# Performance work log

Measured on AMD Instinct MI355X. Metric: run time of the kernel, lower is better.

The kernel has to match this reference:

```python
import jax, jax.numpy as jnp
import numpy as np

EPS = 1e-5

def conv(x, w, groups=1):
    # x: NCHW, w: OIHW, VALID padding, stride 1 (cross-correlation, same as torch conv2d)
    return jax.lax.conv_general_dilated(x, w, (1, 1), 'VALID',
                                        feature_group_count=groups,
                                        dimension_numbers=('NCHW', 'OIHW', 'NCHW'))

def bn(x, g, b, m, v):
    # eval-mode batchnorm with running stats
    scale = (g / jnp.sqrt(v + EPS))[None, :, None, None]
    return (x - m[None, :, None, None]) * scale + b[None, :, None, None]

def xcorr_depthwise(x, k):
    # x: [B,C,Hs,Ws] search, k: [B,C,Hk,Wk] per-sample kernels
    B, C, H, W = x.shape
    xr = x.reshape(1, B * C, H, W)
    kr = k.reshape(B * C, 1, k.shape[2], k.shape[3])
    out = conv(xr, kr, groups=B * C)  # [1, B*C, Ho, Wo]
    return out.reshape(B, C, out.shape[2], out.shape[3])

def setup_inputs() -> dict:
    key = jax.random.key(0)
    ks = jax.random.split(key, 16)
    Cin, Hid, Cout = 256, 256, 20
    inp = {
        'kernel': jax.random.normal(ks[0], (128, Cin, 7, 7), jnp.float32),
        'search': jax.random.normal(ks[1], (128, Cin, 31, 31), jnp.float32),
        'wk': jax.random.normal(ks[2], (Hid, Cin, 3, 3), jnp.float32) * 0.02,
        'gk': jnp.ones((Hid,), jnp.float32),
        'bk': jnp.zeros((Hid,), jnp.float32),
        'mk': jax.random.normal(ks[3], (Hid,), jnp.float32) * 0.1,
        'vk': jax.random.uniform(ks[4], (Hid,), jnp.float32) + 0.5,
        'ws': jax.random.normal(ks[5], (Hid, Cin, 3, 3), jnp.float32) * 0.02,
        'gs': jnp.ones((Hid,), jnp.float32),
        'bs': jnp.zeros((Hid,), jnp.float32),
        'ms': jax.random.normal(ks[6], (Hid,), jnp.float32) * 0.1,
        'vs': jax.random.uniform(ks[7], (Hid,), jnp.float32) + 0.5,
        'wh1': jax.random.normal(ks[8], (Hid, Hid, 1, 1), jnp.float32) * 0.02,
        'gh': jnp.ones((Hid,), jnp.float32),
        'bh': jnp.zeros((Hid,), jnp.float32),
        'mh': jax.random.normal(ks[9], (Hid,), jnp.float32) * 0.1,
        'vh': jax.random.uniform(ks[10], (Hid,), jnp.float32) + 0.5,
        'wh2': jax.random.normal(ks[11], (Cout, Hid, 1, 1), jnp.float32) * 0.02,
        'bh2': jnp.zeros((Cout,), jnp.float32),
    }
    return inp

def reference(kernel, search, wk, gk, bk, mk, vk, ws, gs, bs, ms, vs,
              wh1, gh, bh, mh, vh, wh2, bh2):
    k = jax.nn.relu(bn(conv(kernel, wk), gk, bk, mk, vk))   # [B,256,5,5]
    s = jax.nn.relu(bn(conv(search, ws), gs, bs, ms, vs))   # [B,256,29,29]
    f = xcorr_depthwise(s, k)                               # [B,256,25,25]
    h = jax.nn.relu(bn(conv(f, wh1), gh, bh, mh, vh))
    out = conv(h, wh2) + bh2[None, :, None, None]           # [B,20,25,25]
    return out
```

## Files before the change

kernel.cpp:

```cpp
#include <hip/hip_runtime.h>

typedef __bf16 bf16x8 __attribute__((ext_vector_type(8)));
typedef float floatx4 __attribute__((ext_vector_type(4)));
typedef unsigned short u16;
typedef unsigned int u32;

__device__ __forceinline__ u16 f2bf(float f) {
    union { float f; unsigned int u; } q; q.f = f;
    unsigned int r = q.u + 0x7FFFu + ((q.u >> 16) & 1u);
    return (u16)(r >> 16);
}
__device__ __forceinline__ float bf2f(u16 b) {
    union { unsigned int u; float f; } q; q.u = ((unsigned int)b) << 16;
    return q.f;
}

__device__ __forceinline__ void gl2lds16(const u16* g, u16* l) {
    __builtin_amdgcn_global_load_lds((const __attribute__((address_space(1))) u32*)g,
                                     (__attribute__((address_space(3))) u32*)l, 16, 0, 0);
}


__global__ __launch_bounds__(256) void bn_prep(
    const float* __restrict__ gk, const float* __restrict__ bk,
    const float* __restrict__ mk, const float* __restrict__ vk,
    const float* __restrict__ gs, const float* __restrict__ bs,
    const float* __restrict__ ms, const float* __restrict__ vs,
    const float* __restrict__ gh, const float* __restrict__ bh,
    const float* __restrict__ mh, const float* __restrict__ vh,
    float* __restrict__ par)
{
    int i = threadIdx.x;
    float s;
    s = gk[i] * rsqrtf(vk[i] + 1e-5f); par[0*256+i] = s; par[1*256+i] = bk[i] - mk[i]*s;
    s = gs[i] * rsqrtf(vs[i] + 1e-5f); par[2*256+i] = s; par[3*256+i] = bs[i] - ms[i]*s;
    s = gh[i] * rsqrtf(vh[i] + 1e-5f); par[4*256+i] = s; par[5*256+i] = bh[i] - mh[i]*s;
}

__global__ __launch_bounds__(256) void pack3x3(const float* __restrict__ w, u16* __restrict__ out) {
    int tid = blockIdx.x * 256 + threadIdx.x;
    int o  = tid / 2304;
    int k  = tid - o * 2304;
    int rc = k >> 8;
    int ci = k & 255;
    out[tid] = f2bf(w[o * 2304 + ci * 9 + rc]);
}

__global__ __launch_bounds__(256) void cast_bf16(const float* __restrict__ in, u16* __restrict__ out, int n) {
    int tid = blockIdx.x * 256 + threadIdx.x;
    if (tid < n) out[tid] = f2bf(in[tid]);
}

__global__ __launch_bounds__(256) void nchw2nhwc_t(const float* __restrict__ in, u16* __restrict__ out,
                                                   int HW, int sptiles) {
    __shared__ float tile[64][33];
    int bid = blockIdx.x;
    int st  = bid % sptiles;
    int tmp = bid / sptiles;
    int ct  = tmp & 3;
    int b   = tmp >> 2;
    int sp0 = st * 32, ci0 = ct * 64;
    int t = threadIdx.x;
    int j = t & 31, i8 = t >> 5;
    const float* ip = in + ((size_t)b * 256 + ci0 + i8) * HW + sp0 + j;
#pragma unroll
    for (int k = 0; k < 8; ++k) {
        if (sp0 + j < HW) tile[i8 + k * 8][j] = ip[(size_t)(k * 8) * HW];
    }
    __syncthreads();
    int cl = t & 63, s4 = t >> 6;
#pragma unroll
    for (int k = 0; k < 8; ++k) {
        int spl = s4 + k * 4;
        int sp  = sp0 + spl;
        if (sp < HW) out[((size_t)b * HW + sp) * 256 + ci0 + cl] = f2bf(tile[cl][spl]);
    }
}

__global__ __launch_bounds__(256) void conv_gemm(
    const u16* __restrict__ Ain, const u16* __restrict__ Wpk,
    const float* __restrict__ scale, const float* __restrict__ shift,
    u16* __restrict__ Out,
    int OHW, int OW, int IW, int bstride, int KW, int nrc, int mblocks)
{
    __shared__ u16 Alds[4096];
    __shared__ u16 Blds[4096];

    const int tot = mblocks * 2;
    const int grp = (tot >> 3) << 3;
    const int lid = blockIdx.x;
    const int nid = (lid < grp) ? ((lid & 7) * (grp >> 3) + (lid >> 3)) : lid;
    const int m0 = (nid >> 1) * 128;
    const int n0 = (nid & 1) * 128;

    const int t    = threadIdx.x;
    const int wave = t >> 6;
    const int lane = t & 63;
    const int quad = lane >> 4;
    const int lrow = lane & 15;

    const int koff = (((t & 3) ^ ((t >> 3) & 3)) << 3);
    const int r0 = t >> 2;
    int m_a0 = m0 + r0;
    int b0 = m_a0 / OHW; int rem0 = m_a0 - b0 * OHW; int y0 = rem0 / OW; int x0 = rem0 - y0 * OW;
    int m_a1 = m_a0 + 64;
    int b1 = m_a1 / OHW; int rem1 = m_a1 - b1 * OHW; int y1 = rem1 / OW; int x1 = rem1 - y1 * OW;
    const u16* ag0 = Ain + (size_t)b0 * bstride + (size_t)(y0 * IW + x0) * 256 + koff;
    const u16* ag1 = Ain + (size_t)b1 * bstride + (size_t)(y1 * IW + x1) * 256 + koff;
    const int Ktot = nrc * 256;
    const u16* bg0 = Wpk + (size_t)(n0 + r0) * Ktot + koff;
    const u16* bg1 = bg0 + (size_t)64 * Ktot;

    u16* lA0 = Alds + wave * 512;
    u16* lA1 = Alds + 2048 + wave * 512;
    u16* lB0 = Blds + wave * 512;
    u16* lB1 = Blds + 2048 + wave * 512;

    floatx4 zero = {0.f, 0.f, 0.f, 0.f};
    floatx4 acc[4][4];
#pragma unroll
    for (int i = 0; i < 4; ++i)
#pragma unroll
        for (int j = 0; j < 4; ++j) acc[i][j] = zero;

    const int wr  = (wave >> 1) << 6;
    const int wc  = (wave & 1) << 6;
    const int pos = ((quad ^ ((lrow >> 1) & 3)) << 3);

    const int nchunks = nrc << 3;
    for (int ch = 0; ch < nchunks; ++ch) {
        int rc  = ch >> 3;
        int ci0 = (ch & 7) << 5;
        int rr  = rc / KW;
        int cc  = rc - rr * KW;
        int ao  = (rr * IW + cc) * 256 + ci0;
        int bo  = ch << 5;
        __syncthreads();
        gl2lds16(ag0 + ao, lA0);
        gl2lds16(ag1 + ao, lA1);
        gl2lds16(bg0 + bo, lB0);
        gl2lds16(bg1 + bo, lB1);
        __syncthreads();
        bf16x8 af[4], bfr[4];
#pragma unroll
        for (int mi = 0; mi < 4; ++mi)
            af[mi] = *(const bf16x8*)&Alds[(wr + mi * 16 + lrow) * 32 + pos];
#pragma unroll
        for (int ni = 0; ni < 4; ++ni)
            bfr[ni] = *(const bf16x8*)&Blds[(wc + ni * 16 + lrow) * 32 + pos];
#pragma unroll
        for (int mi = 0; mi < 4; ++mi)
#pragma unroll
            for (int ni = 0; ni < 4; ++ni)
                acc[mi][ni] = __builtin_amdgcn_mfma_f32_16x16x32_bf16(af[mi], bfr[ni], acc[mi][ni], 0, 0, 0);
    }

    float sc[4], sh[4];
#pragma unroll
    for (int ni = 0; ni < 4; ++ni) {
        int gn = n0 + wc + ni * 16 + lrow;
        sc[ni] = scale[gn];
        sh[ni] = shift[gn];
    }
#pragma unroll
    for (int mi = 0; mi < 4; ++mi) {
        int gm = m0 + wr + mi * 16 + (quad << 2);
#pragma unroll
        for (int ri = 0; ri < 4; ++ri) {
            size_t ro = (size_t)(gm + ri) * 256 + n0 + wc + lrow;
#pragma unroll
            for (int ni = 0; ni < 4; ++ni) {
                float v = acc[mi][ni][ri] * sc[ni] + sh[ni];
                v = fmaxf(v, 0.f);
                Out[ro + ni * 16] = f2bf(v);
            }
        }
    }
}

#define NS_BLK 421
__global__ __launch_bounds__(512, 2) void conv_gemm256(
    const u16* __restrict__ AinS, const u16* __restrict__ WpkS,
    const float* __restrict__ parS, u16* __restrict__ OutS,
    const u16* __restrict__ AinK, const u16* __restrict__ WpkK,
    const float* __restrict__ parK, u16* __restrict__ OutK)
{
    __shared__ __align__(16) u16 Alds[2][256][64];
    __shared__ __align__(16) u16 Blds[2][256][64];

    const int Ktot = 2304;
    const int NKT  = 36;
    const int KW   = 3;

    const int lid = blockIdx.x;
    const bool isk = (lid >= NS_BLK);

    int nid;
    if (!isk) {
        const int xcd = lid & 7, sub = lid >> 3;
        nid = (xcd < 5) ? (xcd * 53 + sub) : (265 + (xcd - 5) * 52 + sub);
    } else {
        nid = lid - NS_BLK;
    }
    const int m0 = nid << 8;

    const int OHW     = isk ? 25    : 841;
    const int OW      = isk ? 5     : 29;
    const int IW      = isk ? 7     : 31;
    const int bstride = isk ? 12544 : 246016;
    const int Mtot    = isk ? 3200  : 107648;
    const u16* Ain    = isk ? AinK : AinS;
    const u16* Wpk    = isk ? WpkK : WpkS;
    const float* scale = isk ? parK : parS;
    const float* shift = scale + 256;
    u16* Out          = isk ? OutK : OutS;

    const int t     = threadIdx.x;
    const int wave  = t >> 6;
    const int lane  = t & 63;
    const int lrow  = lane & 15;
    const int lquad = lane >> 4;
    const int wmBase = (wave >> 2) << 7;
    const int wnBase = (wave & 3) << 6;

    const u16* pA[4];
    const u16* pB[4];
#pragma unroll
    for (int j = 0; j < 4; ++j) {
        int u = j * 512 + t;
        int row = u >> 3, slot = u & 7;
        int ko = ((slot ^ (row & 7)) << 3);
        int m = m0 + row; if (m >= Mtot) m = Mtot - 1;
        int b = m / OHW; int rem = m - b * OHW; int y = rem / OW; int x = rem - y * OW;
        pA[j] = Ain + (size_t)b * bstride + (size_t)(y * IW + x) * 256 + ko;
        pB[j] = Wpk + (size_t)row * (size_t)Ktot + ko;
    }

    const int xo0 = ((lquad ^ (lrow & 7)) << 3);
    const int xo1 = xo0 ^ 32;

    floatx4 acc[8][4];
#pragma unroll
    for (int i = 0; i < 8; ++i)
#pragma unroll
        for (int j = 0; j < 4; ++j) acc[i][j] = (floatx4){0.f, 0.f, 0.f, 0.f};

#pragma unroll
    for (int j = 0; j < 4; ++j)
        gl2lds16(pA[j], &Alds[0][0][0] + j * 4096 + wave * 512);
#pragma unroll
    for (int j = 0; j < 4; ++j)
        gl2lds16(pB[j], &Blds[0][0][0] + j * 4096 + wave * 512);
    asm volatile("s_waitcnt vmcnt(0)" ::: "memory");
    __builtin_amdgcn_s_barrier();

#define LOADA(mb) do {                                              \
        const u16* _p = Ab + (wmBase + (mb) * 16 + lrow) * 64;      \
        aF[0][0] = *(const bf16x8*)(_p + xo0);                      \
        aF[0][1] = *(const bf16x8*)(_p + xo1);                      \
        aF[1][0] = *(const bf16x8*)(_p + 1024 + xo0);               \
        aF[1][1] = *(const bf16x8*)(_p + 1024 + xo1);               \
    } while (0)

#define MFMA16(mb) do {                                                                               \
        _Pragma("unroll")                                                                             \
        for (int _n = 0; _n < 4; ++_n) {                                                              \
            acc[(mb)][_n]     = __builtin_amdgcn_mfma_f32_16x16x32_bf16(aF[0][0], bB[_n][0], acc[(mb)][_n], 0, 0, 0);     \
            acc[(mb)][_n]     = __builtin_amdgcn_mfma_f32_16x16x32_bf16(aF[0][1], bB[_n][1], acc[(mb)][_n], 0, 0, 0);     \
            acc[(mb) + 1][_n] = __builtin_amdgcn_mfma_f32_16x16x32_bf16(aF[1][0], bB[_n][0], acc[(mb) + 1][_n], 0, 0, 0); \
            acc[(mb) + 1][_n] = __builtin_amdgcn_mfma_f32_16x16x32_bf16(aF[1][1], bB[_n][1], acc[(mb) + 1][_n], 0, 0, 0); \
        }                                                                                             \
    } while (0)

#define PH_MID() do {                                        \
        __builtin_amdgcn_s_barrier();                        \
        asm volatile("s_waitcnt lgkmcnt(0)" ::: "memory");   \
        __builtin_amdgcn_s_setprio(1);                       \
    } while (0)

#define PH_END() do {                                        \
        __builtin_amdgcn_s_setprio(0);                       \
        __builtin_amdgcn_s_barrier();                        \
    } while (0)

#pragma unroll 2
    for (int kt = 0; kt < NKT; ++kt) {
        const int c = kt & 1;
        const u16* Ab = &Alds[c][0][0];
        const u16* Bb = &Blds[c][0][0];
        u16* An = &Alds[c ^ 1][0][0];
        u16* Bn = &Blds[c ^ 1][0][0];
        const int pf = (kt + 1 < NKT);
        const int kt1 = kt + 1;
        const int rc = kt1 >> 2;
        const int rr = rc / KW;
        const int cc = rc - rr * KW;
        const int aoffA = (rr * IW + cc) * 256 + ((kt1 & 3) << 6);
        const int boffB = kt1 << 6;

        bf16x8 bB[4][2];
        bf16x8 aF[2][2];

#pragma unroll
        for (int ni = 0; ni < 4; ++ni) {
            const u16* _p = Bb + (wnBase + ni * 16 + lrow) * 64;
            bB[ni][0] = *(const bf16x8*)(_p + xo0);
            bB[ni][1] = *(const bf16x8*)(_p + xo1);
        }
        LOADA(0);
        if (pf) {
#pragma unroll
            for (int j = 0; j < 4; ++j)
                gl2lds16(pA[j] + aoffA, An + j * 4096 + wave * 512);
        }
        PH_MID();
        MFMA16(0);
        PH_END();

        LOADA(2);
        if (pf) {
#pragma unroll
            for (int j = 0; j < 4; ++j)
                gl2lds16(pB[j] + boffB, Bn + j * 4096 + wave * 512);
        }
        PH_MID();
        MFMA16(2);
        PH_END();

        LOADA(4);
        PH_MID();
        MFMA16(4);
        PH_END();

        LOADA(6);
        PH_MID();
        MFMA16(6);
        __builtin_amdgcn_s_setprio(0);
        asm volatile("s_waitcnt vmcnt(0)" ::: "memory");
        __builtin_amdgcn_s_barrier();
    }

#undef LOADA
#undef MFMA16
#undef PH_MID
#undef PH_END

    float sc[4], sh[4];
#pragma unroll
    for (int ni = 0; ni < 4; ++ni) {
        int gn = wnBase + ni * 16 + lrow;
        sc[ni] = scale[gn];
        sh[ni] = shift[gn];
    }
#pragma unroll
    for (int mi = 0; mi < 8; ++mi) {
        int gm0 = m0 + wmBase + mi * 16 + (lquad << 2);
#pragma unroll
        for (int ri = 0; ri < 4; ++ri) {
            int gm = gm0 + ri;
            if (gm < Mtot) {
                size_t ro = (size_t)gm * 256 + wnBase + lrow;
#pragma unroll
                for (int ni = 0; ni < 4; ++ni) {
                    float v = acc[mi][ni][ri] * sc[ni] + sh[ni];
                    v = fmaxf(v, 0.f);
                    Out[ro + ni * 16] = f2bf(v);
                }
            }
        }
    }
}

__global__ __launch_bounds__(256) void xcorr(const u16* __restrict__ ss, const u16* __restrict__ kk,
                                             u16* __restrict__ f) {
    int lid = blockIdx.x;
    int bid = (lid & 7) * 400 + (lid >> 3);
    int b = bid / 25, y = bid - b * 25;
    int t = threadIdx.x;
    int cg = (t & 31) << 3;
    int xg = t >> 5;
    const u16* kbase = kk + (size_t)b * 25 * 256 + cg;
    const u16* sbase = ss + (size_t)(b * 29 + y) * 29 * 256 + cg;

    float acc[4][8];
#pragma unroll
    for (int j = 0; j < 4; ++j)
#pragma unroll
        for (int e = 0; e < 8; ++e) acc[j][e] = 0.f;

#pragma unroll
    for (int r = 0; r < 5; ++r) {
        const u16* srow = sbase + (size_t)r * 29 * 256;
#pragma unroll
        for (int c = 0; c < 5; ++c) {
            bf16x8 kv = *(const bf16x8*)(kbase + (r * 5 + c) * 256);
            float kf[8];
#pragma unroll
            for (int e = 0; e < 8; ++e) kf[e] = (float)kv[e];
#pragma unroll
            for (int j = 0; j < 4; ++j) {
                int x = xg + 8 * j;
                if (x < 25) {
                    bf16x8 sv = *(const bf16x8*)(srow + (size_t)(x + c) * 256);
#pragma unroll
                    for (int e = 0; e < 8; ++e) acc[j][e] += (float)sv[e] * kf[e];
                }
            }
        }
    }

    u16* fb = f + (size_t)(b * 25 + y) * 25 * 256 + cg;
#pragma unroll
    for (int j = 0; j < 4; ++j) {
        int x = xg + 8 * j;
        if (x < 25) {
            u16 pk[8];
#pragma unroll
            for (int e = 0; e < 8; ++e) pk[e] = f2bf(acc[j][e]);
            *(bf16x8*)(fb + (size_t)x * 256) = *(const bf16x8*)pk;
        }
    }
}

__global__ __launch_bounds__(256) void head(const u16* __restrict__ h, const float* __restrict__ w2,
                                            const float* __restrict__ b2, float* __restrict__ out) {
    __shared__ __align__(16) u16   hl[25 * 264];
    __shared__ __align__(16) float wl[20 * 260];
    int bid = blockIdx.x;
    int b = bid / 25, y = bid - b * 25;
    int t = threadIdx.x;
    const u16* hrow = h + (size_t)(b * 25 + y) * 25 * 256;
    for (int i = t; i < 800; i += 256) {
        int x = i >> 5, c8 = i & 31;
        *(bf16x8*)&hl[x * 264 + c8 * 8] = *(const bf16x8*)&hrow[i * 8];
    }
    for (int i = t; i < 1280; i += 256) {
        int co = i >> 6, c4 = i & 63;
        *(float4*)&wl[co * 260 + c4 * 4] = *(const float4*)&w2[(size_t)co * 256 + c4 * 4];
    }
    __syncthreads();
    for (int o = t; o < 500; o += 256) {
        int x = o / 20, co = o - x * 20;
        float acc = b2[co];
        const u16* hp = &hl[x * 264];
        const float* wp = &wl[co * 260];
#pragma unroll 4
        for (int k = 0; k < 256; k += 8) {
            bf16x8 hv = *(const bf16x8*)(hp + k);
            float4 w0 = *(const float4*)(wp + k);
            float4 w1 = *(const float4*)(wp + k + 4);
            acc += (float)hv[0] * w0.x + (float)hv[1] * w0.y
                 + (float)hv[2] * w0.z + (float)hv[3] * w0.w
                 + (float)hv[4] * w1.x + (float)hv[5] * w1.y
                 + (float)hv[6] * w1.z + (float)hv[7] * w1.w;
        }
        out[(size_t)((b * 20 + co) * 25 + y) * 25 + x] = acc;
    }
}

#define OFF_SIN  0ull
#define SZ_SIN   62980096ull
#define OFF_KIN  (OFF_SIN + SZ_SIN)
#define SZ_KIN   3211264ull
#define OFF_WKP  (OFF_KIN + SZ_KIN)
#define SZ_WKP   1179648ull
#define OFF_WSP  (OFF_WKP + SZ_WKP)
#define SZ_WSP   1179648ull
#define OFF_WH1P (OFF_WSP + SZ_WSP)
#define SZ_WH1P  131072ull
#define OFF_PAR  (OFF_WH1P + SZ_WH1P)
#define SZ_PAR   8192ull
#define OFF_KK   (OFF_PAR + SZ_PAR)
#define SZ_KK    1638400ull
#define OFF_SS   (OFF_KK + SZ_KK)
#define SZ_SS    55115776ull
#define OFF_F    OFF_SIN
#define OFF_H    OFF_SS

extern "C" void kernel_launch(void* const* d_in, const int* in_sizes, int n_in,
                              void* d_out, int out_size, void* d_ws, size_t ws_size,
                              hipStream_t stream) {
    const float* kin  = (const float*)d_in[0];
    const float* sin_ = (const float*)d_in[1];
    const float* wk   = (const float*)d_in[2];
    const float* gk   = (const float*)d_in[3];
    const float* bk   = (const float*)d_in[4];
    const float* mk   = (const float*)d_in[5];
    const float* vk   = (const float*)d_in[6];
    const float* wsw  = (const float*)d_in[7];
    const float* gs   = (const float*)d_in[8];
    const float* bs   = (const float*)d_in[9];
    const float* ms   = (const float*)d_in[10];
    const float* vs   = (const float*)d_in[11];
    const float* wh1  = (const float*)d_in[12];
    const float* gh   = (const float*)d_in[13];
    const float* bh   = (const float*)d_in[14];
    const float* mh   = (const float*)d_in[15];
    const float* vh   = (const float*)d_in[16];
    const float* wh2  = (const float*)d_in[17];
    const float* bh2  = (const float*)d_in[18];
    float* out = (float*)d_out;

    char* w = (char*)d_ws;
    u16*   SIN  = (u16*)(w + OFF_SIN);
    u16*   KIN  = (u16*)(w + OFF_KIN);
    u16*   WKP  = (u16*)(w + OFF_WKP);
    u16*   WSP  = (u16*)(w + OFF_WSP);
    u16*   WH1P = (u16*)(w + OFF_WH1P);
    float* PAR  = (float*)(w + OFF_PAR);
    u16*   KK   = (u16*)(w + OFF_KK);
    u16*   SS   = (u16*)(w + OFF_SS);
    u16*   F    = (u16*)(w + OFF_F);
    u16*   H    = (u16*)(w + OFF_H);

    bn_prep<<<1, 256, 0, stream>>>(gk, bk, mk, vk, gs, bs, ms, vs, gh, bh, mh, vh, PAR);
    pack3x3<<<2304, 256, 0, stream>>>(wk, WKP);
    pack3x3<<<2304, 256, 0, stream>>>(wsw, WSP);
    cast_bf16<<<256, 256, 0, stream>>>(wh1, WH1P, 65536);
    nchw2nhwc_t<<<128 * 4 * 2, 256, 0, stream>>>(kin, KIN, 49, 2);
    nchw2nhwc_t<<<128 * 4 * 31, 256, 0, stream>>>(sin_, SIN, 961, 31);

    conv_gemm256<<<434, 512, 0, stream>>>(SIN, WSP, PAR + 512, SS,
                                          KIN, WKP, PAR + 0, KK);
    xcorr<<<3200, 256, 0, stream>>>(SS, KK, F);
    conv_gemm<<<1250, 256, 0, stream>>>(F, WH1P, PAR + 1024, PAR + 1280, H,
                                        625, 25, 25, 160000, 1, 1, 625);
    head<<<3200, 256, 0, stream>>>(H, wh2, bh2, out);

    (void)in_sizes; (void)n_in; (void)out_size; (void)ws_size;
}
```

Baseline: 508.9 us.

## Fuse xcorr, 1x1 conv GEMM, and head into one per-row kernel

Merges the depthwise xcorr, the 256x256 1x1 conv with BN/ReLU, and the final 20-channel head into a single kernel per (batch, output row). The xcorr result stays in LDS and feeds MFMA directly, which removes the global round trips for the F and H intermediates and two kernel launches. In exchange, each block reloads the full 256x256 bf16 wh1 weight from global/L2 per row, and the MFMA tile is padded from 25 to 32 rows, wasting some compute.

```diff
diff --git a/kernel.cpp b/kernel.cpp
--- a/kernel.cpp
+++ b/kernel.cpp
@@ -77,107 +77,6 @@
     }
 }
 
-__global__ __launch_bounds__(256) void conv_gemm(
-    const u16* __restrict__ Ain, const u16* __restrict__ Wpk,
-    const float* __restrict__ scale, const float* __restrict__ shift,
-    u16* __restrict__ Out,
-    int OHW, int OW, int IW, int bstride, int KW, int nrc, int mblocks)
-{
-    __shared__ u16 Alds[4096];
-    __shared__ u16 Blds[4096];
-
-    const int tot = mblocks * 2;
-    const int grp = (tot >> 3) << 3;
-    const int lid = blockIdx.x;
-    const int nid = (lid < grp) ? ((lid & 7) * (grp >> 3) + (lid >> 3)) : lid;
-    const int m0 = (nid >> 1) * 128;
-    const int n0 = (nid & 1) * 128;
-
-    const int t    = threadIdx.x;
-    const int wave = t >> 6;
-    const int lane = t & 63;
-    const int quad = lane >> 4;
-    const int lrow = lane & 15;
-
-    const int koff = (((t & 3) ^ ((t >> 3) & 3)) << 3);
-    const int r0 = t >> 2;
-    int m_a0 = m0 + r0;
-    int b0 = m_a0 / OHW; int rem0 = m_a0 - b0 * OHW; int y0 = rem0 / OW; int x0 = rem0 - y0 * OW;
-    int m_a1 = m_a0 + 64;
-    int b1 = m_a1 / OHW; int rem1 = m_a1 - b1 * OHW; int y1 = rem1 / OW; int x1 = rem1 - y1 * OW;
-    const u16* ag0 = Ain + (size_t)b0 * bstride + (size_t)(y0 * IW + x0) * 256 + koff;
-    const u16* ag1 = Ain + (size_t)b1 * bstride + (size_t)(y1 * IW + x1) * 256 + koff;
-    const int Ktot = nrc * 256;
-    const u16* bg0 = Wpk + (size_t)(n0 + r0) * Ktot + koff;
-    const u16* bg1 = bg0 + (size_t)64 * Ktot;
-
-    u16* lA0 = Alds + wave * 512;
-    u16* lA1 = Alds + 2048 + wave * 512;
-    u16* lB0 = Blds + wave * 512;
-    u16* lB1 = Blds + 2048 + wave * 512;
-
-    floatx4 zero = {0.f, 0.f, 0.f, 0.f};
-    floatx4 acc[4][4];
-#pragma unroll
-    for (int i = 0; i < 4; ++i)
-#pragma unroll
-        for (int j = 0; j < 4; ++j) acc[i][j] = zero;
-
-    const int wr  = (wave >> 1) << 6;
-    const int wc  = (wave & 1) << 6;
-    const int pos = ((quad ^ ((lrow >> 1) & 3)) << 3);
-
-    const int nchunks = nrc << 3;
-    for (int ch = 0; ch < nchunks; ++ch) {
-        int rc  = ch >> 3;
-        int ci0 = (ch & 7) << 5;
-        int rr  = rc / KW;
-        int cc  = rc - rr * KW;
-        int ao  = (rr * IW + cc) * 256 + ci0;
-        int bo  = ch << 5;
-        __syncthreads();
-        gl2lds16(ag0 + ao, lA0);
-        gl2lds16(ag1 + ao, lA1);
-        gl2lds16(bg0 + bo, lB0);
-        gl2lds16(bg1 + bo, lB1);
-        __syncthreads();
-        bf16x8 af[4], bfr[4];
-#pragma unroll
-        for (int mi = 0; mi < 4; ++mi)
-            af[mi] = *(const bf16x8*)&Alds[(wr + mi * 16 + lrow) * 32 + pos];
-#pragma unroll
-        for (int ni = 0; ni < 4; ++ni)
-            bfr[ni] = *(const bf16x8*)&Blds[(wc + ni * 16 + lrow) * 32 + pos];
-#pragma unroll
-        for (int mi = 0; mi < 4; ++mi)
-#pragma unroll
-            for (int ni = 0; ni < 4; ++ni)
-                acc[mi][ni] = __builtin_amdgcn_mfma_f32_16x16x32_bf16(af[mi], bfr[ni], acc[mi][ni], 0, 0, 0);
-    }
-
-    float sc[4], sh[4];
-#pragma unroll
-    for (int ni = 0; ni < 4; ++ni) {
-        int gn = n0 + wc + ni * 16 + lrow;
-        sc[ni] = scale[gn];
-        sh[ni] = shift[gn];
-    }
-#pragma unroll
-    for (int mi = 0; mi < 4; ++mi) {
-        int gm = m0 + wr + mi * 16 + (quad << 2);
-#pragma unroll
-        for (int ri = 0; ri < 4; ++ri) {
-            size_t ro = (size_t)(gm + ri) * 256 + n0 + wc + lrow;
-#pragma unroll
-            for (int ni = 0; ni < 4; ++ni) {
-                float v = acc[mi][ni][ri] * sc[ni] + sh[ni];
-                v = fmaxf(v, 0.f);
-                Out[ro + ni * 16] = f2bf(v);
-            }
-        }
-    }
-}
-
 #define NS_BLK 421
 __global__ __launch_bounds__(512, 2) void conv_gemm256(
     const u16* __restrict__ AinS, const u16* __restrict__ WpkS,
@@ -371,88 +270,137 @@
     }
 }
 
-__global__ __launch_bounds__(256) void xcorr(const u16* __restrict__ ss, const u16* __restrict__ kk,
-                                             u16* __restrict__ f) {
+__global__ __launch_bounds__(256) void xcorr_head(
+    const u16* __restrict__ ss, const u16* __restrict__ kk,
+    const u16* __restrict__ w1, const float* __restrict__ parh,
+    const float* __restrict__ w2, const float* __restrict__ b2,
+    float* __restrict__ out)
+{
+    __shared__ __align__(16) u16   Flds[32 * 264];
+    __shared__ __align__(16) float wl[20 * 260];
+
     int lid = blockIdx.x;
     int bid = (lid & 7) * 400 + (lid >> 3);
     int b = bid / 25, y = bid - b * 25;
     int t = threadIdx.x;
-    int cg = (t & 31) << 3;
-    int xg = t >> 5;
-    const u16* kbase = kk + (size_t)b * 25 * 256 + cg;
-    const u16* sbase = ss + (size_t)(b * 29 + y) * 29 * 256 + cg;
-
-    float acc[4][8];
-#pragma unroll
-    for (int j = 0; j < 4; ++j)
-#pragma unroll
-        for (int e = 0; e < 8; ++e) acc[j][e] = 0.f;
-
-#pragma unroll
-    for (int r = 0; r < 5; ++r) {
-        const u16* srow = sbase + (size_t)r * 29 * 256;
-#pragma unroll
-        for (int c = 0; c < 5; ++c) {
-            bf16x8 kv = *(const bf16x8*)(kbase + (r * 5 + c) * 256);
-            float kf[8];
-#pragma unroll
-            for (int e = 0; e < 8; ++e) kf[e] = (float)kv[e];
-#pragma unroll
-            for (int j = 0; j < 4; ++j) {
-                int x = xg + 8 * j;
-                if (x < 25) {
-                    bf16x8 sv = *(const bf16x8*)(srow + (size_t)(x + c) * 256);
-#pragma unroll
-                    for (int e = 0; e < 8; ++e) acc[j][e] += (float)sv[e] * kf[e];
-                }
-            }
-        }
-    }
-
-    u16* fb = f + (size_t)(b * 25 + y) * 25 * 256 + cg;
-#pragma unroll
-    for (int j = 0; j < 4; ++j) {
-        int x = xg + 8 * j;
-        if (x < 25) {
-            u16 pk[8];
-#pragma unroll
-            for (int e = 0; e < 8; ++e) pk[e] = f2bf(acc[j][e]);
-            *(bf16x8*)(fb + (size_t)x * 256) = *(const bf16x8*)pk;
-        }
-    }
-}
-
-__global__ __launch_bounds__(256) void head(const u16* __restrict__ h, const float* __restrict__ w2,
-                                            const float* __restrict__ b2, float* __restrict__ out) {
-    __shared__ __align__(16) u16   hl[25 * 264];
-    __shared__ __align__(16) float wl[20 * 260];
-    int bid = blockIdx.x;
-    int b = bid / 25, y = bid - b * 25;
-    int t = threadIdx.x;
-    const u16* hrow = h + (size_t)(b * 25 + y) * 25 * 256;
-    for (int i = t; i < 800; i += 256) {
-        int x = i >> 5, c8 = i & 31;
-        *(bf16x8*)&hl[x * 264 + c8 * 8] = *(const bf16x8*)&hrow[i * 8];
-    }
+
     for (int i = t; i < 1280; i += 256) {
         int co = i >> 6, c4 = i & 63;
         *(float4*)&wl[co * 260 + c4 * 4] = *(const float4*)&w2[(size_t)co * 256 + c4 * 4];
     }
+
+    {
+        int cg = (t & 31) << 3;
+        int xg = t >> 5;
+        const u16* kbase = kk + (size_t)b * 25 * 256 + cg;
+        const u16* sbase = ss + (size_t)(b * 29 + y) * 29 * 256 + cg;
+
+        float acc[4][8];
+#pragma unroll
+        for (int j = 0; j < 4; ++j)
+#pragma unroll
+            for (int e = 0; e < 8; ++e) acc[j][e] = 0.f;
+
+#pragma unroll
+        for (int r = 0; r < 5; ++r) {
+            const u16* srow = sbase + (size_t)r * 29 * 256;
+#pragma unroll
+            for (int c = 0; c < 5; ++c) {
+                bf16x8 kv = *(const bf16x8*)(kbase + (r * 5 + c) * 256);
+                float kf[8];
+#pragma unroll
+                for (int e = 0; e < 8; ++e) kf[e] = (float)kv[e];
+#pragma unroll
+                for (int j = 0; j < 4; ++j) {
+                    int x = xg + 8 * j;
+                    if (x < 25) {
+                        bf16x8 sv = *(const bf16x8*)(srow + (size_t)(x + c) * 256);
+#pragma unroll
+                        for (int e = 0; e < 8; ++e) acc[j][e] += (float)sv[e] * kf[e];
+                    }
+                }
+            }
+        }
+#pragma unroll
+        for (int j = 0; j < 4; ++j) {
+            int x = xg + 8 * j;
+            if (x < 25) {
+                u16 pk[8];
+#pragma unroll
+                for (int e = 0; e < 8; ++e) pk[e] = f2bf(acc[j][e]);
+                *(bf16x8*)&Flds[x * 264 + cg] = *(const bf16x8*)pk;
+            }
+        }
+    }
     __syncthreads();
+
+    {
+        int wave = t >> 6, lane = t & 63;
+        int lr = lane & 15, lq = lane >> 4;
+        int nb = wave << 6;
+
+        floatx4 hacc[2][4];
+#pragma unroll
+        for (int i = 0; i < 2; ++i)
+#pragma unroll
+            for (int j = 0; j < 4; ++j) hacc[i][j] = (floatx4){0.f, 0.f, 0.f, 0.f};
+
+#pragma unroll
+        for (int ks = 0; ks < 8; ++ks) {
+            int ko = ks * 32 + lq * 8;
+            bf16x8 a0 = *(const bf16x8*)&Flds[(lr)      * 264 + ko];
+            bf16x8 a1 = *(const bf16x8*)&Flds[(16 + lr) * 264 + ko];
+            bf16x8 bv[4];
+#pragma unroll
+            for (int ni = 0; ni < 4; ++ni)
+                bv[ni] = *(const bf16x8*)&w1[(size_t)(nb + ni * 16 + lr) * 256 + ko];
+#pragma unroll
+            for (int ni = 0; ni < 4; ++ni) {
+                hacc[0][ni] = __builtin_amdgcn_mfma_f32_16x16x32_bf16(a0, bv[ni], hacc[0][ni], 0, 0, 0);
+                hacc[1][ni] = __builtin_amdgcn_mfma_f32_16x16x32_bf16(a1, bv[ni], hacc[1][ni], 0, 0, 0);
+            }
+        }
+
+        float sc[4], sh[4];
+#pragma unroll
+        for (int ni = 0; ni < 4; ++ni) {
+            int gn = nb + ni * 16 + lr;
+            sc[ni] = parh[gn];
+            sh[ni] = parh[256 + gn];
+        }
+        __syncthreads();
+#pragma unroll
+        for (int mt = 0; mt < 2; ++mt) {
+#pragma unroll
+            for (int reg = 0; reg < 4; ++reg) {
+                int row = mt * 16 + lq * 4 + reg;
+                if (row < 25) {
+#pragma unroll
+                    for (int ni = 0; ni < 4; ++ni) {
+                        float v = hacc[mt][ni][reg] * sc[ni] + sh[ni];
+                        v = fmaxf(v, 0.f);
+                        Flds[row * 264 + nb + ni * 16 + lr] = f2bf(v);
+                    }
+                }
+            }
+        }
+    }
+    __syncthreads();
+
     for (int o = t; o < 500; o += 256) {
         int x = o / 20, co = o - x * 20;
         float acc = b2[co];
-        const u16* hp = &hl[x * 264];
+        const u16* hp = &Flds[x * 264];
         const float* wp = &wl[co * 260];
 #pragma unroll 4
         for (int k = 0; k < 256; k += 8) {
             bf16x8 hv = *(const bf16x8*)(hp + k);
             float4 w0 = *(const float4*)(wp + k);
-            float4 w1 = *(const float4*)(wp + k + 4);
+            float4 w1v = *(const float4*)(wp + k + 4);
             acc += (float)hv[0] * w0.x + (float)hv[1] * w0.y
                  + (float)hv[2] * w0.z + (float)hv[3] * w0.w
-                 + (float)hv[4] * w1.x + (float)hv[5] * w1.y
-                 + (float)hv[6] * w1.z + (float)hv[7] * w1.w;
+                 + (float)hv[4] * w1v.x + (float)hv[5] * w1v.y
+                 + (float)hv[6] * w1v.z + (float)hv[7] * w1v.w;
         }
         out[(size_t)((b * 20 + co) * 25 + y) * 25 + x] = acc;
     }
@@ -474,8 +422,6 @@
 #define SZ_KK    1638400ull
 #define OFF_SS   (OFF_KK + SZ_KK)
 #define SZ_SS    55115776ull
-#define OFF_F    OFF_SIN
-#define OFF_H    OFF_SS
 
 extern "C" void kernel_launch(void* const* d_in, const int* in_sizes, int n_in,
                               void* d_out, int out_size, void* d_ws, size_t ws_size,
@@ -510,8 +456,6 @@
     float* PAR  = (float*)(w + OFF_PAR);
     u16*   KK   = (u16*)(w + OFF_KK);
     u16*   SS   = (u16*)(w + OFF_SS);
-    u16*   F    = (u16*)(w + OFF_F);
-    u16*   H    = (u16*)(w + OFF_H);
 
     bn_prep<<<1, 256, 0, stream>>>(gk, bk, mk, vk, gs, bs, ms, vs, gh, bh, mh, vh, PAR);
     pack3x3<<<2304, 256, 0, stream>>>(wk, WKP);
@@ -522,10 +466,7 @@
 
     conv_gemm256<<<434, 512, 0, stream>>>(SIN, WSP, PAR + 512, SS,
                                           KIN, WKP, PAR + 0, KK);
-    xcorr<<<3200, 256, 0, stream>>>(SS, KK, F);
-    conv_gemm<<<1250, 256, 0, stream>>>(F, WH1P, PAR + 1024, PAR + 1280, H,
-                                        625, 25, 25, 160000, 1, 1, 625);
-    head<<<3200, 256, 0, stream>>>(H, wh2, bh2, out);
+    xcorr_head<<<3200, 256, 0, stream>>>(SS, KK, WH1P, PAR + 1024, wh2, bh2, out);
 
     (void)in_sizes; (void)n_in; (void)out_size; (void)ws_size;
 }
```

Result: slower. 534.1 us (+4.9%).
